# Performance work log

Measured on AMD Instinct MI355X. Metric: run time of the kernel, lower is better.

Reference implementation:

```python
import jax, jax.numpy as jnp
import numpy as np

D = 256      # dim
H = 8        # num_heads
HD = D // H  # head dim
P = 256      # patch_size
B = 4        # num clouds
L = 32768    # points per cloud (divisible by P)
N = B * L
MLP = int(D * 2.0)
PEH = max(32, D // 4)
EPS = 1e-5


def setup_inputs() -> dict:
    key = jax.random.key(0)
    ks = jax.random.split(key, 20)
    s = 0.02
    w = lambda k, shp: jax.random.normal(k, shp, jnp.float32) * s
    inp = {
        "feats": jax.random.normal(ks[0], (N, D), jnp.float32),
        "coord": jax.random.uniform(ks[1], (N, 3), jnp.float32),
        "lengths": jnp.full((B,), L, jnp.int32),
        # CoordPositionalEncoding: Linear(3,PEH) -> ReLU -> Linear(PEH,D)
        "pe_w1": w(ks[2], (3, PEH)), "pe_b1": jnp.zeros((PEH,), jnp.float32),
        "pe_w2": w(ks[3], (PEH, D)), "pe_b2": jnp.zeros((D,), jnp.float32),
        "pre_g": jnp.ones((D,), jnp.float32), "pre_b": jnp.zeros((D,), jnp.float32),
        # block: norm1 + MHA + norm2 + MLP
        "n1_g": jnp.ones((D,), jnp.float32), "n1_b": jnp.zeros((D,), jnp.float32),
        "wqkv": w(ks[4], (D, 3 * D)), "bqkv": jnp.zeros((3 * D,), jnp.float32),
        "wo": w(ks[5], (D, D)), "bo": jnp.zeros((D,), jnp.float32),
        "n2_g": jnp.ones((D,), jnp.float32), "n2_b": jnp.zeros((D,), jnp.float32),
        "m_w1": w(ks[6], (D, MLP)), "m_b1": jnp.zeros((MLP,), jnp.float32),
        "m_w2": w(ks[7], (MLP, D)), "m_b2": jnp.zeros((D,), jnp.float32),
        # global_gate: Linear(2D,D)->ReLU->Linear(D,D)->Sigmoid
        "gg_w1": w(ks[8], (2 * D, D)), "gg_b1": jnp.zeros((D,), jnp.float32),
        "gg_w2": w(ks[9], (D, D)), "gg_b2": jnp.zeros((D,), jnp.float32),
        # fuse: Linear(2D,D)->ReLU->Linear(D,D)
        "f_w1": w(ks[10], (2 * D, D)), "f_b1": jnp.zeros((D,), jnp.float32),
        "f_w2": w(ks[11], (D, D)), "f_b2": jnp.zeros((D,), jnp.float32),
    }
    return inp


def _ln(x, g, b):
    m = x.mean(-1, keepdims=True)
    v = jnp.mean((x - m) ** 2, -1, keepdims=True)
    return (x - m) * jax.lax.rsqrt(v + EPS) * g + b


def _sgca(feats, coord, lengths,
          pe_w1, pe_b1, pe_w2, pe_b2, pre_g, pre_b,
          n1_g, n1_b, wqkv, bqkv, wo, bo, n2_g, n2_b,
          m_w1, m_b1, m_w2, m_b2,
          gg_w1, gg_b1, gg_w2, gg_b2, f_w1, f_b1, f_w2, f_b2):
    Bn = lengths.shape[0]
    Ln = feats.shape[0] // Bn  # equal-length clouds

    def cloud(f, c):  # f: [L, D], c: [L, 3]
        # positional encoding (per-cloud centered / max-abs scaled coords)
        cc = c - c.mean(0, keepdims=True)
        scale = jnp.clip(jnp.abs(cc).max(0, keepdims=True), 1e-6)
        pe = jax.nn.relu((cc / scale) @ pe_w1 + pe_b1) @ pe_w2 + pe_b2
        x = _ln(f + pe, pre_g, pre_b)
        # serialization order from min-max normalized coords
        cn = c - c.min(0, keepdims=True)
        cn = cn / jnp.clip(cn.max(0, keepdims=True), 1e-6)
        key = cn[:, 0] + 2.17 * cn[:, 1] + 3.31 * cn[:, 2]
        order = jnp.argsort(key)
        xs = x[order].reshape(-1, P, D)  # [NP, P, D] block-diagonal windows
        # attention block (pre-norm MHA + residual)
        h = _ln(xs, n1_g, n1_b)
        qkv = h @ wqkv + bqkv
        q = qkv[..., :D].reshape(-1, P, H, HD)
        k = qkv[..., D:2 * D].reshape(-1, P, H, HD)
        v = qkv[..., 2 * D:].reshape(-1, P, H, HD)
        scores = jnp.einsum('nphd,nqhd->nhpq', q, k) / np.sqrt(HD).astype(np.float32)
        a = jax.nn.softmax(scores, axis=-1)
        o = jnp.einsum('nhpq,nqhd->nphd', a, v).reshape(-1, P, D)
        xs = xs + (o @ wo + bo)
        # MLP + residual
        xs = xs + (jax.nn.gelu(_ln(xs, n2_g, n2_b) @ m_w1 + m_b1, approximate=False) @ m_w2 + m_b2)
        # undo serialization
        xo = xs.reshape(-1, D)[jnp.argsort(order)]
        # global token gate/fuse
        gt = jnp.broadcast_to(xo.mean(0, keepdims=True), xo.shape)
        gate = jax.nn.sigmoid(jax.nn.relu(jnp.concatenate([f, gt], -1) @ gg_w1 + gg_b1) @ gg_w2 + gg_b2)
        fused = jax.nn.relu(jnp.concatenate([xo, gt], -1) @ f_w1 + f_b1) @ f_w2 + f_b2
        return f + gate * fused

    out = jax.vmap(cloud)(feats.reshape(Bn, Ln, D), coord.reshape(Bn, Ln, 3))
    return out.reshape(-1, D)


def reference(feats, coord, lengths,
              pe_w1, pe_b1, pe_w2, pe_b2, pre_g, pre_b,
              n1_g, n1_b, wqkv, bqkv, wo, bo, n2_g, n2_b,
              m_w1, m_b1, m_w2, m_b2,
              gg_w1, gg_b1, gg_w2, gg_b2, f_w1, f_b1, f_w2, f_b2):
    return _sgca(feats, coord, lengths,
                 pe_w1, pe_b1, pe_w2, pe_b2, pre_g, pre_b,
                 n1_g, n1_b, wqkv, bqkv, wo, bo, n2_g, n2_b,
                 m_w1, m_b1, m_w2, m_b2,
                 gg_w1, gg_b1, gg_w2, gg_b2, f_w1, f_b1, f_w2, f_b2)
```

## Files before the change

### kernel.cpp

```cpp
#include <hip/hip_runtime.h>
#include <hip/hip_bf16.h>
#include <math.h>

#define D_DIM 256
#define NHEAD 8
#define HDIM 32
#define PATCH 256
#define NCLOUD 4
#define LPC 32768
#define NTOT (NCLOUD * LPC)
#define MLPD 512
#define PEHID 64
#define LN_EPS 1e-5f
#define NCHUNK 4
#define CROWS (NTOT / NCHUNK)

typedef unsigned long long u64;
typedef unsigned short u16;
typedef short bf16x8 __attribute__((ext_vector_type(8)));
typedef float f32x4 __attribute__((ext_vector_type(4)));

__device__ __forceinline__ u16 f2bf(float x) {
  unsigned u = __float_as_uint(x);
  u += 0x7fffu + ((u >> 16) & 1u);
  return (u16)(u >> 16);
}
__device__ __forceinline__ float bf2f(u16 u) {
  return __uint_as_float(((unsigned)u) << 16);
}

__device__ __forceinline__ void gload_lds16(const u16* g, u16* l) {
  __builtin_amdgcn_global_load_lds((const __attribute__((address_space(1))) void*)g,
                                   (__attribute__((address_space(3))) void*)l, 16, 0, 0);
}

__global__ __launch_bounds__(256) void stats_kernel(const float* __restrict__ coord,
                                                    float* __restrict__ stats) {
  const int c = blockIdx.x, t = threadIdx.x;
  float sm[3] = {0.f, 0.f, 0.f};
  float mn[3] = {1e30f, 1e30f, 1e30f};
  float mx[3] = {-1e30f, -1e30f, -1e30f};
  const float* cp = coord + (size_t)c * LPC * 3;
  for (int i = t; i < LPC; i += 256) {
#pragma unroll
    for (int a = 0; a < 3; a++) {
      float v = cp[(size_t)i * 3 + a];
      sm[a] += v;
      mn[a] = fminf(mn[a], v);
      mx[a] = fmaxf(mx[a], v);
    }
  }
  __shared__ float sb[256];
  float rsum[3], rmn[3], rmx[3];
#pragma unroll
  for (int a = 0; a < 3; a++) {
    sb[t] = sm[a]; __syncthreads();
    for (int s = 128; s > 0; s >>= 1) { if (t < s) sb[t] += sb[t + s]; __syncthreads(); }
    rsum[a] = sb[0]; __syncthreads();
    sb[t] = mn[a]; __syncthreads();
    for (int s = 128; s > 0; s >>= 1) { if (t < s) sb[t] = fminf(sb[t], sb[t + s]); __syncthreads(); }
    rmn[a] = sb[0]; __syncthreads();
    sb[t] = mx[a]; __syncthreads();
    for (int s = 128; s > 0; s >>= 1) { if (t < s) sb[t] = fmaxf(sb[t], sb[t + s]); __syncthreads(); }
    rmx[a] = sb[0]; __syncthreads();
  }
  if (t == 0) {
    float* st = stats + c * 16;
#pragma unroll
    for (int a = 0; a < 3; a++) {
      float mean = rsum[a] / (float)LPC;
      st[a] = mean;
      st[3 + a] = fmaxf(fmaxf(rmx[a] - mean, mean - rmn[a]), 1e-6f);
      st[6 + a] = rmn[a];
      st[9 + a] = fmaxf(rmx[a] - rmn[a], 1e-6f);
    }
  }
}

__global__ __launch_bounds__(256) void key_kernel(const float* __restrict__ coord,
                                                  const float* __restrict__ stats,
                                                  u64* __restrict__ keys) {
#pragma clang fp contract(off)
  const int g = blockIdx.x * 256 + threadIdx.x;
  const int c = g >> 15;
  const float* st = stats + c * 16;
  float k0 = (coord[(size_t)g * 3 + 0] - st[6]) / st[9];
  float k1 = (coord[(size_t)g * 3 + 1] - st[7]) / st[10];
  float k2 = (coord[(size_t)g * 3 + 2] - st[8]) / st[11];
  float key = k0 + 2.17f * k1;
  key = key + 3.31f * k2;
  keys[g] = ((u64)__float_as_uint(key) << 32) | (unsigned)(g & (LPC - 1));
}

__global__ __launch_bounds__(1024) void sort_local_kernel(u64* __restrict__ keys) {
  __shared__ u64 s[4096];
  const int base = blockIdx.x * 4096;
  const int t = threadIdx.x;
  for (int i = t; i < 4096; i += 1024) s[i] = keys[base + i];
  __syncthreads();
  for (int k = 2; k <= 4096; k <<= 1) {
    for (int j = k >> 1; j > 0; j >>= 1) {
      for (int p = t; p < 2048; p += 1024) {
        int i = ((p & ~(j - 1)) << 1) | (p & (j - 1));
        int l = i | j;
        bool asc = (((base + i) & (LPC - 1)) & k) == 0;
        u64 a = s[i], bb = s[l];
        if (asc ? (a > bb) : (a < bb)) { s[i] = bb; s[l] = a; }
      }
      __syncthreads();
    }
  }
  for (int i = t; i < 4096; i += 1024) keys[base + i] = s[i];
}

__global__ __launch_bounds__(256) void sort_global_kernel(u64* __restrict__ keys, int k, int j) {
  int p = blockIdx.x * 256 + threadIdx.x;
  int i = ((p & ~(j - 1)) << 1) | (p & (j - 1));
  int l = i | j;
  bool asc = ((i & (LPC - 1)) & k) == 0;
  u64 a = keys[i], b = keys[l];
  if (asc ? (a > b) : (a < b)) { keys[i] = b; keys[l] = a; }
}

__global__ __launch_bounds__(1024) void sort_finish_kernel(u64* __restrict__ keys, int k) {
  __shared__ u64 s[4096];
  const int base = blockIdx.x * 4096;
  const int t = threadIdx.x;
  for (int i = t; i < 4096; i += 1024) s[i] = keys[base + i];
  __syncthreads();
  for (int j = 2048; j > 0; j >>= 1) {
    for (int p = t; p < 2048; p += 1024) {
      int i = ((p & ~(j - 1)) << 1) | (p & (j - 1));
      int l = i | j;
      bool asc = (((base + i) & (LPC - 1)) & k) == 0;
      u64 a = s[i], bb = s[l];
      if (asc ? (a > bb) : (a < bb)) { s[i] = bb; s[l] = a; }
    }
    __syncthreads();
  }
  for (int i = t; i < 4096; i += 1024) keys[base + i] = s[i];
}

__global__ __launch_bounds__(256) void rank_kernel(const u64* __restrict__ keys,
                                                   int* __restrict__ order,
                                                   int* __restrict__ rank) {
  const int g = blockIdx.x * 256 + threadIdx.x;
  const int src = (int)(unsigned)(keys[g] & 0xffffffffULL) + (g & ~(LPC - 1));
  order[g] = src;
  rank[src] = g;
}

__global__ __launch_bounds__(256) void wtrans_kernel(const float* __restrict__ src,
                                                     u16* __restrict__ dst, int R, int C) {
  __shared__ float t[32][33];
  const int bx = blockIdx.x * 32, by = blockIdx.y * 32;
  const int lc = threadIdx.x & 31, lr = threadIdx.x >> 5;
  for (int i = 0; i < 32; i += 8) t[lr + i][lc] = src[(size_t)(by + lr + i) * C + bx + lc];
  __syncthreads();
  for (int i = 0; i < 32; i += 8)
    dst[(size_t)(bx + lr + i) * R + by + lc] = f2bf(t[lc][lr + i]);
}

__global__ __launch_bounds__(256) void h_kernel(const float* __restrict__ coord,
                                                const float* __restrict__ stats,
                                                const float* __restrict__ pw1,
                                                const float* __restrict__ pb1,
                                                u16* __restrict__ H) {
  const int idx = blockIdx.x * 256 + threadIdx.x;
  const int row = idx >> 6, j = idx & 63;
  const int c = row >> 15;
  const float* st = stats + c * 16;
  float s0 = (coord[(size_t)row * 3 + 0] - st[0]) / st[3];
  float s1 = (coord[(size_t)row * 3 + 1] - st[1]) / st[4];
  float s2 = (coord[(size_t)row * 3 + 2] - st[2]) / st[5];
  float h = pb1[j] + s0 * pw1[j] + s1 * pw1[64 + j] + s2 * pw1[128 + j];
  H[idx] = f2bf(fmaxf(h, 0.f));
}

__global__ __launch_bounds__(256) void add_ln_kernel(const float* __restrict__ feats,
                                                     const u16* __restrict__ pe,
                                                     const int* __restrict__ rank,
                                                     const float* __restrict__ g,
                                                     const float* __restrict__ b,
                                                     float* __restrict__ xs) {
  const int row = blockIdx.x * 4 + (threadIdx.x >> 6);
  const int lane = threadIdx.x & 63;
  float4 f = *(const float4*)(feats + (size_t)row * 256 + lane * 4);
  ushort4 p = *(const ushort4*)(pe + (size_t)row * 256 + lane * 4);
  float v0 = f.x + bf2f(p.x), v1 = f.y + bf2f(p.y);
  float v2 = f.z + bf2f(p.z), v3 = f.w + bf2f(p.w);
  float s = v0 + v1 + v2 + v3;
#pragma unroll
  for (int o = 32; o > 0; o >>= 1) s += __shfl_xor(s, o);
  float mean = s * (1.f / 256.f);
  float d0 = v0 - mean, d1 = v1 - mean, d2 = v2 - mean, d3 = v3 - mean;
  float ss = d0 * d0 + d1 * d1 + d2 * d2 + d3 * d3;
#pragma unroll
  for (int o = 32; o > 0; o >>= 1) ss += __shfl_xor(ss, o);
  float inv = 1.f / sqrtf(ss * (1.f / 256.f) + LN_EPS);
  float4 gv = *(const float4*)(g + lane * 4);
  float4 bv = *(const float4*)(b + lane * 4);
  int dst = rank[row];
  float4 o4;
  o4.x = d0 * inv * gv.x + bv.x; o4.y = d1 * inv * gv.y + bv.y;
  o4.z = d2 * inv * gv.z + bv.z; o4.w = d3 * inv * gv.w + bv.w;
  *(float4*)(xs + (size_t)dst * 256 + lane * 4) = o4;
}

__global__ __launch_bounds__(256) void ln_bf16_kernel(const float* __restrict__ in,
                                                      const float* __restrict__ g,
                                                      const float* __restrict__ b,
                                                      u16* __restrict__ out) {
  const int row = blockIdx.x * 4 + (threadIdx.x >> 6);
  const int lane = threadIdx.x & 63;
  float4 v = *(const float4*)(in + (size_t)row * 256 + lane * 4);
  float s = v.x + v.y + v.z + v.w;
#pragma unroll
  for (int o = 32; o > 0; o >>= 1) s += __shfl_xor(s, o);
  float mean = s * (1.f / 256.f);
  float d0 = v.x - mean, d1 = v.y - mean, d2 = v.z - mean, d3 = v.w - mean;
  float ss = d0 * d0 + d1 * d1 + d2 * d2 + d3 * d3;
#pragma unroll
  for (int o = 32; o > 0; o >>= 1) ss += __shfl_xor(ss, o);
  float inv = 1.f / sqrtf(ss * (1.f / 256.f) + LN_EPS);
  float4 gv = *(const float4*)(g + lane * 4);
  float4 bv = *(const float4*)(b + lane * 4);
  ushort4 o4;
  o4.x = f2bf(d0 * inv * gv.x + bv.x); o4.y = f2bf(d1 * inv * gv.y + bv.y);
  o4.z = f2bf(d2 * inv * gv.z + bv.z); o4.w = f2bf(d3 * inv * gv.w + bv.w);
  *(ushort4*)(out + (size_t)row * 256 + lane * 4) = o4;
}

template <int K, int ACT, int MODE, bool EXTRA>
__global__ __launch_bounds__(256, 4) void mfma_gemm(const u16* __restrict__ A,
                                                    const u16* __restrict__ Wt,
                                                    const float* __restrict__ bias,
                                                    const float* __restrict__ extra,
                                                    void* __restrict__ Cout, int Ko) {
  __shared__ __align__(16) u16 Al[128 * 32];
  __shared__ __align__(16) u16 Bl[128 * 32];
  const int tid = threadIdx.x;
  const int lane = tid & 63, wave = tid >> 6;
  const int wr = wave >> 1, wc = wave & 1;
  const int l15 = lane & 15, l4 = lane >> 4;
  const size_t row0 = (size_t)blockIdx.y * 128;
  const int col0 = blockIdx.x * 128;
  const int q0 = wave * 64 + lane;
  const int q1 = q0 + 256;
  const u16* gA0 = A + (row0 + (q0 >> 2)) * K + (q0 & 3) * 8;
  const u16* gA1 = A + (row0 + (q1 >> 2)) * K + (q1 & 3) * 8;
  const u16* gB0 = Wt + (size_t)(col0 + (q0 >> 2)) * K + (q0 & 3) * 8;
  const u16* gB1 = Wt + (size_t)(col0 + (q1 >> 2)) * K + (q1 & 3) * 8;
  u16* lA0 = Al + wave * 512;
  u16* lA1 = Al + 2048 + wave * 512;
  u16* lB0 = Bl + wave * 512;
  u16* lB1 = Bl + 2048 + wave * 512;
  f32x4 acc[4][4];
#pragma unroll
  for (int i = 0; i < 4; i++)
#pragma unroll
    for (int j = 0; j < 4; j++) acc[i][j] = f32x4{0.f, 0.f, 0.f, 0.f};
#pragma unroll 1
  for (int k0 = 0; k0 < K; k0 += 32) {
    gload_lds16(gA0 + k0, lA0);
    gload_lds16(gA1 + k0, lA1);
    gload_lds16(gB0 + k0, lB0);
    gload_lds16(gB1 + k0, lB1);
    __syncthreads();
    bf16x8 af[4], bfr[4];
#pragma unroll
    for (int rb = 0; rb < 4; rb++)
      af[rb] = *(const bf16x8*)&Al[(wr * 64 + rb * 16 + l15) * 32 + l4 * 8];
#pragma unroll
    for (int cb = 0; cb < 4; cb++)
      bfr[cb] = *(const bf16x8*)&Bl[(wc * 64 + cb * 16 + l15) * 32 + l4 * 8];
#pragma unroll
    for (int rb = 0; rb < 4; rb++)
#pragma unroll
      for (int cb = 0; cb < 4; cb++)
        acc[rb][cb] = __builtin_amdgcn_mfma_f32_16x16x32_bf16(af[rb], bfr[cb], acc[rb][cb], 0, 0, 0);
    __syncthreads();
  }
#pragma unroll
  for (int rb = 0; rb < 4; rb++)
#pragma unroll
    for (int cb = 0; cb < 4; cb++)
#pragma unroll
      for (int r = 0; r < 4; r++) {
        size_t row = row0 + wr * 64 + rb * 16 + l4 * 4 + r;
        int col = col0 + wc * 64 + cb * 16 + l15;
        float v = acc[rb][cb][r] + bias[col];
        if (EXTRA) v += extra[((int)(row >> 15)) * 256 + col];
        if (ACT == 1) v = fmaxf(v, 0.f);
        else if (ACT == 2) v = 0.5f * v * (1.f + erff(v * 0.70710678118654752440f));
        else if (ACT == 3) v = 1.f / (1.f + __expf(-v));
        size_t o = row * (size_t)Ko + col;
        if (MODE == 0) ((float*)Cout)[o] = v;
        else if (MODE == 1) ((float*)Cout)[o] += v;
        else ((u16*)Cout)[o] = f2bf(v);
      }
}

template <int K, int EPI>
__global__ __launch_bounds__(256, 3) void mfma_row_gemm(const u16* __restrict__ A,
                                                        const u16* __restrict__ Wt,
                                                        const float* __restrict__ bias,
                                                        float* __restrict__ xs,
                                                        u16* __restrict__ hout,
                                                        const int* __restrict__ order,
                                                        const float* __restrict__ g,
                                                        const float* __restrict__ b) {
  __shared__ __align__(16) u16 Al[64 * 32];
  __shared__ __align__(16) u16 Bl[256 * 32];
  __shared__ float reds[2][4][64];
  const int tid = threadIdx.x;
  const int lane = tid & 63, wave = tid >> 6;
  const int l15 = lane & 15, l4 = lane >> 4;
  const size_t row0 = (size_t)blockIdx.x * 64;
  const u16* gA = A + (row0 + (tid >> 2)) * K + (tid & 3) * 8;
  u16* lA = Al + wave * 512;
  const u16* gB[4];
  u16* lB[4];
#pragma unroll
  for (int s = 0; s < 4; s++) {
    int q = s * 256 + tid;
    gB[s] = Wt + (size_t)(q >> 2) * K + (q & 3) * 8;
    lB[s] = Bl + s * 2048 + wave * 512;
  }
  f32x4 acc[4][4];
#pragma unroll
  for (int i = 0; i < 4; i++)
#pragma unroll
    for (int j = 0; j < 4; j++) acc[i][j] = f32x4{0.f, 0.f, 0.f, 0.f};
#pragma unroll 1
  for (int k0 = 0; k0 < K; k0 += 32) {
    gload_lds16(gA + k0, lA);
#pragma unroll
    for (int s = 0; s < 4; s++) gload_lds16(gB[s] + k0, lB[s]);
    __syncthreads();
    bf16x8 af[4], bfr[4];
#pragma unroll
    for (int rb = 0; rb < 4; rb++)
      af[rb] = *(const bf16x8*)&Al[(rb * 16 + l15) * 32 + l4 * 8];
#pragma unroll
    for (int cb = 0; cb < 4; cb++)
      bfr[cb] = *(const bf16x8*)&Bl[(wave * 64 + cb * 16 + l15) * 32 + l4 * 8];
#pragma unroll
    for (int rb = 0; rb < 4; rb++)
#pragma unroll
      for (int cb = 0; cb < 4; cb++)
        acc[rb][cb] = __builtin_amdgcn_mfma_f32_16x16x32_bf16(af[rb], bfr[cb], acc[rb][cb], 0, 0, 0);
    __syncthreads();
  }
#pragma unroll
  for (int rb = 0; rb < 4; rb++)
#pragma unroll
    for (int cb = 0; cb < 4; cb++)
#pragma unroll
      for (int r = 0; r < 4; r++) {
        size_t row = row0 + rb * 16 + l4 * 4 + r;
        int col = wave * 64 + cb * 16 + l15;
        size_t o = row * 256 + col;
        float t = xs[o] + acc[rb][cb][r] + bias[col];
        xs[o] = t;
        acc[rb][cb][r] = t;
      }
  if (EPI == 1) {
    float ps[4][4];
#pragma unroll
    for (int rb = 0; rb < 4; rb++)
#pragma unroll
      for (int r = 0; r < 4; r++) {
        float v = acc[rb][0][r] + acc[rb][1][r] + acc[rb][2][r] + acc[rb][3][r];
#pragma unroll
        for (int oo = 1; oo < 16; oo <<= 1) v += __shfl_xor(v, oo);
        ps[rb][r] = v;
      }
    if (l15 == 0)
#pragma unroll
      for (int rb = 0; rb < 4; rb++)
#pragma unroll
        for (int r = 0; r < 4; r++) reds[0][wave][rb * 16 + l4 * 4 + r] = ps[rb][r];
    __syncthreads();
    float mean[4][4];
#pragma unroll
    for (int rb = 0; rb < 4; rb++)
#pragma unroll
      for (int r = 0; r < 4; r++) {
        int ri = rb * 16 + l4 * 4 + r;
        mean[rb][r] = (reds[0][0][ri] + reds[0][1][ri] + reds[0][2][ri] + reds[0][3][ri]) *
                      (1.f / 256.f);
      }
#pragma unroll
    for (int rb = 0; rb < 4; rb++)
#pragma unroll
      for (int r = 0; r < 4; r++) {
        float d0 = acc[rb][0][r] - mean[rb][r], d1 = acc[rb][1][r] - mean[rb][r];
        float d2 = acc[rb][2][r] - mean[rb][r], d3 = acc[rb][3][r] - mean[rb][r];
        float v = d0 * d0 + d1 * d1 + d2 * d2 + d3 * d3;
#pragma unroll
        for (int oo = 1; oo < 16; oo <<= 1) v += __shfl_xor(v, oo);
        ps[rb][r] = v;
      }
    if (l15 == 0)
#pragma unroll
      for (int rb = 0; rb < 4; rb++)
#pragma unroll
        for (int r = 0; r < 4; r++) reds[1][wave][rb * 16 + l4 * 4 + r] = ps[rb][r];
    __syncthreads();
#pragma unroll
    for (int rb = 0; rb < 4; rb++)
#pragma unroll
      for (int r = 0; r < 4; r++) {
        int ri = rb * 16 + l4 * 4 + r;
        float var = (reds[1][0][ri] + reds[1][1][ri] + reds[1][2][ri] + reds[1][3][ri]) *
                    (1.f / 256.f);
        float inv = 1.f / sqrtf(var + LN_EPS);
        size_t row = row0 + ri;
#pragma unroll
        for (int cb = 0; cb < 4; cb++) {
          int col = wave * 64 + cb * 16 + l15;
          hout[row * 256 + col] =
              f2bf((acc[rb][cb][r] - mean[rb][r]) * inv * g[col] + b[col]);
        }
      }
  } else {
#pragma unroll
    for (int rb = 0; rb < 4; rb++)
#pragma unroll
      for (int r = 0; r < 4; r++) {
        size_t row = row0 + rb * 16 + l4 * 4 + r;
        size_t dst = (size_t)order[row];
#pragma unroll
        for (int cb = 0; cb < 4; cb++) {
          int col = wave * 64 + cb * 16 + l15;
          hout[dst * 256 + col] = f2bf(acc[rb][cb][r]);
        }
      }
  }
}

__global__ __launch_bounds__(256, 3) void tail_kernel(
    const float* __restrict__ feats, const u16* __restrict__ xobf,
    const u16* __restrict__ ggw1T, const u16* __restrict__ fw1T,
    const u16* __restrict__ ggw2T, const u16* __restrict__ fw2T,
    const float* __restrict__ ggt, const float* __restrict__ fgt,
    const float* __restrict__ b1g, const float* __restrict__ b1f,
    const float* __restrict__ b2g, const float* __restrict__ b2f,
    float* __restrict__ out) {
  __shared__ __align__(16) u16 g1l[32 * 264];
  __shared__ __align__(16) u16 u1l[32 * 264];
  __shared__ __align__(16) u16 Bst[256 * 32];
  __shared__ __align__(16) u16 Ast[32 * 32];
  const int tid = threadIdx.x;
  const int lane = tid & 63, wave = tid >> 6;
  const int l15 = lane & 15, l4 = lane >> 4;
  const size_t row0 = (size_t)blockIdx.x * 32;
  const int cloud = (int)(row0 >> 15);
  f32x4 acc[2][4];
#pragma unroll
  for (int i = 0; i < 2; i++)
#pragma unroll
    for (int j = 0; j < 4; j++) acc[i][j] = f32x4{0.f, 0.f, 0.f, 0.f};
#pragma unroll 1
  for (int k0 = 0; k0 < 256; k0 += 32) {
#pragma unroll
    for (int s = 0; s < 4; s++) {
      int q = s * 256 + tid;
      gload_lds16(ggw1T + (size_t)(q >> 2) * 256 + k0 + (q & 3) * 8,
                  Bst + s * 2048 + wave * 512);
    }
    {
      int r = tid >> 3, c4 = (tid & 7) * 4;
      float4 v = *(const float4*)(feats + (row0 + r) * 256 + k0 + c4);
      ushort4 o4; o4.x = f2bf(v.x); o4.y = f2bf(v.y); o4.z = f2bf(v.z); o4.w = f2bf(v.w);
      *(ushort4*)&Ast[r * 32 + c4] = o4;
    }
    __syncthreads();
    bf16x8 af[2];
#pragma unroll
    for (int rb = 0; rb < 2; rb++)
      af[rb] = *(const bf16x8*)&Ast[(rb * 16 + l15) * 32 + l4 * 8];
#pragma unroll
    for (int cb = 0; cb < 4; cb++) {
      bf16x8 bf = *(const bf16x8*)&Bst[(wave * 64 + cb * 16 + l15) * 32 + l4 * 8];
#pragma unroll
      for (int rb = 0; rb < 2; rb++)
        acc[rb][cb] = __builtin_amdgcn_mfma_f32_16x16x32_bf16(af[rb], bf, acc[rb][cb], 0, 0, 0);
    }
    __syncthreads();
  }
#pragma unroll
  for (int rb = 0; rb < 2; rb++)
#pragma unroll
    for (int cb = 0; cb < 4; cb++)
#pragma unroll
      for (int r = 0; r < 4; r++) {
        int row = rb * 16 + l4 * 4 + r;
        int col = wave * 64 + cb * 16 + l15;
        float v = acc[rb][cb][r] + b1g[col] + ggt[cloud * 256 + col];
        g1l[row * 264 + col] = f2bf(fmaxf(v, 0.f));
      }
#pragma unroll
  for (int i = 0; i < 2; i++)
#pragma unroll
    for (int j = 0; j < 4; j++) acc[i][j] = f32x4{0.f, 0.f, 0.f, 0.f};
#pragma unroll 1
  for (int k0 = 0; k0 < 256; k0 += 32) {
    __syncthreads();
#pragma unroll
    for (int s = 0; s < 4; s++) {
      int q = s * 256 + tid;
      gload_lds16(fw1T + (size_t)(q >> 2) * 256 + k0 + (q & 3) * 8,
                  Bst + s * 2048 + wave * 512);
    }
    if (tid < 128) {
      int q = tid;
      gload_lds16(xobf + (row0 + (q >> 2)) * 256 + k0 + (q & 3) * 8, Ast + wave * 512);
    }
    __syncthreads();
    bf16x8 af[2];
#pragma unroll
    for (int rb = 0; rb < 2; rb++)
      af[rb] = *(const bf16x8*)&Ast[(rb * 16 + l15) * 32 + l4 * 8];
#pragma unroll
    for (int cb = 0; cb < 4; cb++) {
      bf16x8 bf = *(const bf16x8*)&Bst[(wave * 64 + cb * 16 + l15) * 32 + l4 * 8];
#pragma unroll
      for (int rb = 0; rb < 2; rb++)
        acc[rb][cb] = __builtin_amdgcn_mfma_f32_16x16x32_bf16(af[rb], bf, acc[rb][cb], 0, 0, 0);
    }
  }
#pragma unroll
  for (int rb = 0; rb < 2; rb++)
#pragma unroll
    for (int cb = 0; cb < 4; cb++)
#pragma unroll
      for (int r = 0; r < 4; r++) {
        int row = rb * 16 + l4 * 4 + r;
        int col = wave * 64 + cb * 16 + l15;
        float v = acc[rb][cb][r] + b1f[col] + fgt[cloud * 256 + col];
        u1l[row * 264 + col] = f2bf(fmaxf(v, 0.f));
      }
#pragma unroll
  for (int i = 0; i < 2; i++)
#pragma unroll
    for (int j = 0; j < 4; j++) acc[i][j] = f32x4{0.f, 0.f, 0.f, 0.f};
#pragma unroll 1
  for (int k0 = 0; k0 < 256; k0 += 32) {
    __syncthreads();
#pragma unroll
    for (int s = 0; s < 4; s++) {
      int q = s * 256 + tid;
      gload_lds16(ggw2T + (size_t)(q >> 2) * 256 + k0 + (q & 3) * 8,
                  Bst + s * 2048 + wave * 512);
    }
    __syncthreads();
    bf16x8 af[2];
#pragma unroll
    for (int rb = 0; rb < 2; rb++)
      af[rb] = *(const bf16x8*)&g1l[(rb * 16 + l15) * 264 + k0 + l4 * 8];
#pragma unroll
    for (int cb = 0; cb < 4; cb++) {
      bf16x8 bf = *(const bf16x8*)&Bst[(wave * 64 + cb * 16 + l15) * 32 + l4 * 8];
#pragma unroll
      for (int rb = 0; rb < 2; rb++)
        acc[rb][cb] = __builtin_amdgcn_mfma_f32_16x16x32_bf16(af[rb], bf, acc[rb][cb], 0, 0, 0);
    }
  }
  float sg[2][4][4];
#pragma unroll
  for (int rb = 0; rb < 2; rb++)
#pragma unroll
    for (int cb = 0; cb < 4; cb++)
#pragma unroll
      for (int r = 0; r < 4; r++) {
        int col = wave * 64 + cb * 16 + l15;
        sg[rb][cb][r] = 1.f / (1.f + __expf(-(acc[rb][cb][r] + b2g[col])));
      }
#pragma unroll
  for (int i = 0; i < 2; i++)
#pragma unroll
    for (int j = 0; j < 4; j++) acc[i][j] = f32x4{0.f, 0.f, 0.f, 0.f};
#pragma unroll 1
  for (int k0 = 0; k0 < 256; k0 += 32) {
    __syncthreads();
#pragma unroll
    for (int s = 0; s < 4; s++) {
      int q = s * 256 + tid;
      gload_lds16(fw2T + (size_t)(q >> 2) * 256 + k0 + (q & 3) * 8,
                  Bst + s * 2048 + wave * 512);
    }
    __syncthreads();
    bf16x8 af[2];
#pragma unroll
    for (int rb = 0; rb < 2; rb++)
      af[rb] = *(const bf16x8*)&u1l[(rb * 16 + l15) * 264 + k0 + l4 * 8];
#pragma unroll
    for (int cb = 0; cb < 4; cb++) {
      bf16x8 bf = *(const bf16x8*)&Bst[(wave * 64 + cb * 16 + l15) * 32 + l4 * 8];
#pragma unroll
      for (int rb = 0; rb < 2; rb++)
        acc[rb][cb] = __builtin_amdgcn_mfma_f32_16x16x32_bf16(af[rb], bf, acc[rb][cb], 0, 0, 0);
    }
  }
#pragma unroll
  for (int rb = 0; rb < 2; rb++)
#pragma unroll
    for (int cb = 0; cb < 4; cb++)
#pragma unroll
      for (int r = 0; r < 4; r++) {
        size_t row = row0 + rb * 16 + l4 * 4 + r;
        int col = wave * 64 + cb * 16 + l15;
        size_t o = row * 256 + col;
        out[o] = feats[o] + sg[rb][cb][r] * (acc[rb][cb][r] + b2f[col]);
      }
}

__global__ __launch_bounds__(256, 3) void attn_mfma_kernel(const u16* __restrict__ qkv,
                                                           u16* __restrict__ ao) {
  __shared__ __align__(16) u16 VT[32 * 264];
  __shared__ __align__(16) u16 Pl[4][16 * 264];
  const int w = blockIdx.x, h = blockIdx.y;
  const int tid = threadIdx.x;
  const int lane = tid & 63, wave = tid >> 6;
  const int l15 = lane & 15, l4 = lane >> 4;
  const size_t base = (size_t)w * PATCH;
  {
    const u16* vrow = qkv + (base + tid) * 768 + 512 + h * HDIM;
#pragma unroll
    for (int d4 = 0; d4 < 8; d4++) {
      ushort4 v4 = *(const ushort4*)(vrow + d4 * 4);
      VT[(d4 * 4 + 0) * 264 + tid] = v4.x;
      VT[(d4 * 4 + 1) * 264 + tid] = v4.y;
      VT[(d4 * 4 + 2) * 264 + tid] = v4.z;
      VT[(d4 * 4 + 3) * 264 + tid] = v4.w;
    }
  }
  __syncthreads();
  u16* Pw = &Pl[wave][0];
  const float scale = 0.17677669529663687f;
  const f32x4 zero = {0.f, 0.f, 0.f, 0.f};
  for (int qt = 0; qt < 4; qt++) {
    const int qbase = wave * 64 + qt * 16;
    bf16x8 qf = *(const bf16x8*)(qkv + (base + qbase + l15) * 768 + h * HDIM + l4 * 8);
    f32x4 s[16];
#pragma unroll
    for (int kt = 0; kt < 16; kt++) {
      bf16x8 kf = *(const bf16x8*)(qkv + (base + kt * 16 + l15) * 768 + 256 + h * HDIM + l4 * 8);
      s[kt] = __builtin_amdgcn_mfma_f32_16x16x32_bf16(kf, qf, zero, 0, 0, 0);
    }
    float m = -1e30f;
#pragma unroll
    for (int kt = 0; kt < 16; kt++)
#pragma unroll
      for (int r = 0; r < 4; r++) { s[kt][r] *= scale; m = fmaxf(m, s[kt][r]); }
    m = fmaxf(m, __shfl_xor(m, 16));
    m = fmaxf(m, __shfl_xor(m, 32));
    float lsum = 0.f;
#pragma unroll
    for (int kt = 0; kt < 16; kt++) {
      float p0 = __expf(s[kt][0] - m), p1 = __expf(s[kt][1] - m);
      float p2 = __expf(s[kt][2] - m), p3 = __expf(s[kt][3] - m);
      lsum += (p0 + p1) + (p2 + p3);
      ushort4 pw4;
      pw4.x = f2bf(p0); pw4.y = f2bf(p1); pw4.z = f2bf(p2); pw4.w = f2bf(p3);
      *(ushort4*)&Pw[l15 * 264 + kt * 16 + l4 * 4] = pw4;
    }
    lsum += __shfl_xor(lsum, 16);
    lsum += __shfl_xor(lsum, 32);
    f32x4 o0 = zero, o1 = zero;
#pragma unroll
    for (int kc = 0; kc < 8; kc++) {
      bf16x8 pf = *(const bf16x8*)&Pw[l15 * 264 + kc * 32 + l4 * 8];
      bf16x8 va = *(const bf16x8*)&VT[l15 * 264 + kc * 32 + l4 * 8];
      bf16x8 vb = *(const bf16x8*)&VT[(16 + l15) * 264 + kc * 32 + l4 * 8];
      o0 = __builtin_amdgcn_mfma_f32_16x16x32_bf16(va, pf, o0, 0, 0, 0);
      o1 = __builtin_amdgcn_mfma_f32_16x16x32_bf16(vb, pf, o1, 0, 0, 0);
    }
    float inv = 1.f / lsum;
    u16* op = ao + (base + qbase + l15) * D_DIM + h * HDIM;
    ushort4 w0, w1;
    w0.x = f2bf(o0[0] * inv); w0.y = f2bf(o0[1] * inv);
    w0.z = f2bf(o0[2] * inv); w0.w = f2bf(o0[3] * inv);
    w1.x = f2bf(o1[0] * inv); w1.y = f2bf(o1[1] * inv);
    w1.z = f2bf(o1[2] * inv); w1.w = f2bf(o1[3] * inv);
    *(ushort4*)(op + l4 * 4) = w0;
    *(ushort4*)(op + 16 + l4 * 4) = w1;
  }
}

__global__ __launch_bounds__(256) void gt_partial_kernel(const float* __restrict__ xs,
                                                         float* __restrict__ part) {
  const int s = blockIdx.x, c = blockIdx.y;
  const int t = threadIdx.x;
  float acc = 0.f;
  const size_t base = (size_t)c * LPC + (size_t)s * 256;
  for (int r = 0; r < 256; r++) acc += xs[(base + r) * D_DIM + t];
  part[(size_t)(c * 128 + s) * D_DIM + t] = acc;
}

__global__ __launch_bounds__(256) void gt_reduce_kernel(const float* __restrict__ part,
                                                        float* __restrict__ gt) {
  const int c = blockIdx.x, t = threadIdx.x;
  float s = 0.f;
  for (int i = 0; i < 128; i++) s += part[(size_t)(c * 128 + i) * D_DIM + t];
  gt[c * D_DIM + t] = s * (1.f / (float)LPC);
}

__global__ __launch_bounds__(256) void pervec_kernel(const float* __restrict__ gt,
                                                     const float* __restrict__ ggw1,
                                                     const float* __restrict__ fw1,
                                                     float* __restrict__ ggt,
                                                     float* __restrict__ fgt) {
  const int c = blockIdx.x, which = blockIdx.y;
  const int t = threadIdx.x;
  const float* W = which ? fw1 : ggw1;
  float* o = which ? fgt : ggt;
  __shared__ float g[D_DIM];
  g[t] = gt[c * D_DIM + t];
  __syncthreads();
  float acc = 0.f;
#pragma unroll 8
  for (int k = 0; k < D_DIM; k++) acc += g[k] * W[(size_t)(256 + k) * D_DIM + t];
  o[c * D_DIM + t] = acc;
}

extern "C" void kernel_launch(void* const* d_in, const int* in_sizes, int n_in,
                              void* d_out, int out_size, void* d_ws, size_t ws_size,
                              hipStream_t stream) {
  const float* feats = (const float*)d_in[0];
  const float* coord = (const float*)d_in[1];
  const float* pe_w1 = (const float*)d_in[3];
  const float* pe_b1 = (const float*)d_in[4];
  const float* pe_w2 = (const float*)d_in[5];
  const float* pe_b2 = (const float*)d_in[6];
  const float* pre_g = (const float*)d_in[7];
  const float* pre_b = (const float*)d_in[8];
  const float* n1_g = (const float*)d_in[9];
  const float* n1_b = (const float*)d_in[10];
  const float* wqkv = (const float*)d_in[11];
  const float* bqkv = (const float*)d_in[12];
  const float* wo = (const float*)d_in[13];
  const float* bo = (const float*)d_in[14];
  const float* n2_g = (const float*)d_in[15];
  const float* n2_b = (const float*)d_in[16];
  const float* m_w1 = (const float*)d_in[17];
  const float* m_b1 = (const float*)d_in[18];
  const float* m_w2 = (const float*)d_in[19];
  const float* m_b2 = (const float*)d_in[20];
  const float* gg_w1 = (const float*)d_in[21];
  const float* gg_b1 = (const float*)d_in[22];
  const float* gg_w2 = (const float*)d_in[23];
  const float* gg_b2 = (const float*)d_in[24];
  const float* f_w1 = (const float*)d_in[25];
  const float* f_b1 = (const float*)d_in[26];
  const float* f_w2 = (const float*)d_in[27];
  const float* f_b2 = (const float*)d_in[28];
  float* out = (float*)d_out;

  char* ws = (char*)d_ws;
  float* xs = (float*)(ws);
  u16* hbuf = (u16*)(ws + 134217728);
  u16* qkvchunk = (u16*)(ws + 201326592);
  u16* aochunk = (u16*)(ws + 251658240);
  u16* tbuf = (u16*)(ws + 268435456);
  u16* Hbuf = (u16*)(ws + 268435456);
  u16* xobf = (u16*)(ws + 201326592);
  size_t off = 301989888;
  u64* keybuf = (u64*)(ws + off); off += (size_t)NTOT * 8;
  int* orderbuf = (int*)(ws + off); off += (size_t)NTOT * 4;
  int* rankbuf = (int*)(ws + off); off += (size_t)NTOT * 4;
  float* statsbuf = (float*)(ws + off); off += 4096;
  float* gtpart = (float*)(ws + off); off += (size_t)NCLOUD * 128 * D_DIM * 4;
  float* gtbuf = (float*)(ws + off); off += 4096;
  float* ggtbuf = (float*)(ws + off); off += 4096;
  float* fgtbuf = (float*)(ws + off); off += 4096;
  u16* wqkvT = (u16*)(ws + off); off += 768 * 256 * 2;
  u16* woT = (u16*)(ws + off); off += 256 * 256 * 2;
  u16* mw1T = (u16*)(ws + off); off += 512 * 256 * 2;
  u16* mw2T = (u16*)(ws + off); off += 256 * 512 * 2;
  u16* ggw1T = (u16*)(ws + off); off += 256 * 256 * 2;
  u16* ggw2T = (u16*)(ws + off); off += 256 * 256 * 2;
  u16* fw1T = (u16*)(ws + off); off += 256 * 256 * 2;
  u16* fw2T = (u16*)(ws + off); off += 256 * 256 * 2;
  u16* pw2T = (u16*)(ws + off); off += 64 * 256 * 2;

  stats_kernel<<<NCLOUD, 256, 0, stream>>>(coord, statsbuf);
  key_kernel<<<NTOT / 256, 256, 0, stream>>>(coord, statsbuf, keybuf);
  sort_local_kernel<<<NTOT / 4096, 1024, 0, stream>>>(keybuf);
  for (int k = 8192; k <= 32768; k <<= 1) {
    for (int j = k >> 1; j >= 4096; j >>= 1)
      sort_global_kernel<<<NTOT / 512, 256, 0, stream>>>(keybuf, k, j);
    sort_finish_kernel<<<NTOT / 4096, 1024, 0, stream>>>(keybuf, k);
  }
  rank_kernel<<<NTOT / 256, 256, 0, stream>>>(keybuf, orderbuf, rankbuf);
  wtrans_kernel<<<dim3(24, 8), 256, 0, stream>>>(wqkv, wqkvT, 256, 768);
  wtrans_kernel<<<dim3(8, 8), 256, 0, stream>>>(wo, woT, 256, 256);
  wtrans_kernel<<<dim3(16, 8), 256, 0, stream>>>(m_w1, mw1T, 256, 512);
  wtrans_kernel<<<dim3(8, 16), 256, 0, stream>>>(m_w2, mw2T, 512, 256);
  wtrans_kernel<<<dim3(8, 8), 256, 0, stream>>>(gg_w1, ggw1T, 256, 256);
  wtrans_kernel<<<dim3(8, 8), 256, 0, stream>>>(gg_w2, ggw2T, 256, 256);
  wtrans_kernel<<<dim3(8, 8), 256, 0, stream>>>(f_w1, fw1T, 256, 256);
  wtrans_kernel<<<dim3(8, 8), 256, 0, stream>>>(f_w2, fw2T, 256, 256);
  wtrans_kernel<<<dim3(8, 2), 256, 0, stream>>>(pe_w2, pw2T, 64, 256);
  h_kernel<<<NTOT * 64 / 256, 256, 0, stream>>>(coord, statsbuf, pe_w1, pe_b1, Hbuf);
  mfma_gemm<64, 0, 2, false><<<dim3(2, NTOT / 128), 256, 0, stream>>>(
      Hbuf, pw2T, pe_b2, nullptr, hbuf, 256);
  add_ln_kernel<<<NTOT / 4, 256, 0, stream>>>(feats, hbuf, rankbuf, pre_g, pre_b, xs);
  ln_bf16_kernel<<<NTOT / 4, 256, 0, stream>>>(xs, n1_g, n1_b, hbuf);
  for (int ch = 0; ch < NCHUNK; ch++) {
    const size_t ro = (size_t)ch * CROWS;
    mfma_gemm<256, 0, 2, false><<<dim3(6, CROWS / 128), 256, 0, stream>>>(
        hbuf + ro * 256, wqkvT, bqkv, nullptr, qkvchunk, 768);
    attn_mfma_kernel<<<dim3(CROWS / PATCH, NHEAD), 256, 0, stream>>>(qkvchunk, aochunk);
    mfma_row_gemm<256, 1><<<CROWS / 64, 256, 0, stream>>>(
        aochunk, woT, bo, xs + ro * 256, hbuf + ro * 256, nullptr, n2_g, n2_b);
  }
  for (int ch = 0; ch < NCHUNK; ch++) {
    const size_t ro = (size_t)ch * CROWS;
    mfma_gemm<256, 2, 2, false><<<dim3(MLPD / 128, CROWS / 128), 256, 0, stream>>>(
        hbuf + ro * 256, mw1T, m_b1, nullptr, tbuf, 512);
    mfma_row_gemm<512, 2><<<CROWS / 64, 256, 0, stream>>>(
        tbuf, mw2T, m_b2, xs + ro * 256, xobf, orderbuf + ro, nullptr, nullptr);
  }
  gt_partial_kernel<<<dim3(128, NCLOUD), 256, 0, stream>>>(xs, gtpart);
  gt_reduce_kernel<<<NCLOUD, 256, 0, stream>>>(gtpart, gtbuf);
  pervec_kernel<<<dim3(NCLOUD, 2), 256, 0, stream>>>(gtbuf, gg_w1, f_w1, ggtbuf, fgtbuf);
  tail_kernel<<<NTOT / 32, 256, 0, stream>>>(feats, xobf, ggw1T, fw1T, ggw2T, fw2T,
                                             ggtbuf, fgtbuf, gg_b1, f_b1, gg_b2, f_b2, out);
  (void)in_sizes; (void)n_in; (void)out_size; (void)ws_size;
}
```

Baseline: 1.359 ms.

## Load tail GEMM operands directly from global memory, dropping LDS staging

The four chained GEMMs in the tail kernel now read weight and activation fragments straight from global memory into registers instead of staging them through shared-memory tiles. This removes the per-k-step barriers and the LDS buffers, lowering LDS use so more blocks may fit per CU. A single barrier is added before the second-stage GEMMs so the intermediate LDS tiles are complete before use. In exchange, each wave issues uncoalesced 16-byte global loads with no prefetch and relies on L2/L1 caching of the shared weights.

```diff
diff --git a/kernel.cpp b/kernel.cpp
--- a/kernel.cpp
+++ b/kernel.cpp
@@ -450,45 +450,39 @@
     float* __restrict__ out) {
   __shared__ __align__(16) u16 g1l[32 * 264];
   __shared__ __align__(16) u16 u1l[32 * 264];
-  __shared__ __align__(16) u16 Bst[256 * 32];
-  __shared__ __align__(16) u16 Ast[32 * 32];
   const int tid = threadIdx.x;
   const int lane = tid & 63, wave = tid >> 6;
   const int l15 = lane & 15, l4 = lane >> 4;
   const size_t row0 = (size_t)blockIdx.x * 32;
   const int cloud = (int)(row0 >> 15);
   f32x4 acc[2][4];
+
 #pragma unroll
   for (int i = 0; i < 2; i++)
 #pragma unroll
     for (int j = 0; j < 4; j++) acc[i][j] = f32x4{0.f, 0.f, 0.f, 0.f};
 #pragma unroll 1
   for (int k0 = 0; k0 < 256; k0 += 32) {
-#pragma unroll
-    for (int s = 0; s < 4; s++) {
-      int q = s * 256 + tid;
-      gload_lds16(ggw1T + (size_t)(q >> 2) * 256 + k0 + (q & 3) * 8,
-                  Bst + s * 2048 + wave * 512);
-    }
-    {
-      int r = tid >> 3, c4 = (tid & 7) * 4;
-      float4 v = *(const float4*)(feats + (row0 + r) * 256 + k0 + c4);
-      ushort4 o4; o4.x = f2bf(v.x); o4.y = f2bf(v.y); o4.z = f2bf(v.z); o4.w = f2bf(v.w);
-      *(ushort4*)&Ast[r * 32 + c4] = o4;
-    }
-    __syncthreads();
     bf16x8 af[2];
 #pragma unroll
-    for (int rb = 0; rb < 2; rb++)
-      af[rb] = *(const bf16x8*)&Ast[(rb * 16 + l15) * 32 + l4 * 8];
+    for (int rb = 0; rb < 2; rb++) {
+      const float* fp = feats + (row0 + rb * 16 + l15) * 256 + k0 + l4 * 8;
+      float4 v0 = *(const float4*)(fp);
+      float4 v1 = *(const float4*)(fp + 4);
+      ushort4 h0, h1;
+      h0.x = f2bf(v0.x); h0.y = f2bf(v0.y); h0.z = f2bf(v0.z); h0.w = f2bf(v0.w);
+      h1.x = f2bf(v1.x); h1.y = f2bf(v1.y); h1.z = f2bf(v1.z); h1.w = f2bf(v1.w);
+      union { ushort4 u4[2]; bf16x8 b8; } cvt;
+      cvt.u4[0] = h0; cvt.u4[1] = h1;
+      af[rb] = cvt.b8;
+    }
 #pragma unroll
     for (int cb = 0; cb < 4; cb++) {
-      bf16x8 bf = *(const bf16x8*)&Bst[(wave * 64 + cb * 16 + l15) * 32 + l4 * 8];
+      bf16x8 bf = *(const bf16x8*)(ggw1T + (size_t)(wave * 64 + cb * 16 + l15) * 256 + k0 + l4 * 8);
 #pragma unroll
       for (int rb = 0; rb < 2; rb++)
         acc[rb][cb] = __builtin_amdgcn_mfma_f32_16x16x32_bf16(af[rb], bf, acc[rb][cb], 0, 0, 0);
     }
-    __syncthreads();
   }
 #pragma unroll
   for (int rb = 0; rb < 2; rb++)
@@ -507,25 +501,13 @@
     for (int j = 0; j < 4; j++) acc[i][j] = f32x4{0.f, 0.f, 0.f, 0.f};
 #pragma unroll 1
   for (int k0 = 0; k0 < 256; k0 += 32) {
-    __syncthreads();
-#pragma unroll
-    for (int s = 0; s < 4; s++) {
-      int q = s * 256 + tid;
-      gload_lds16(fw1T + (size_t)(q >> 2) * 256 + k0 + (q & 3) * 8,
-                  Bst + s * 2048 + wave * 512);
-    }
-    if (tid < 128) {
-      int q = tid;
-      gload_lds16(xobf + (row0 + (q >> 2)) * 256 + k0 + (q & 3) * 8, Ast + wave * 512);
-    }
-    __syncthreads();
     bf16x8 af[2];
 #pragma unroll
     for (int rb = 0; rb < 2; rb++)
-      af[rb] = *(const bf16x8*)&Ast[(rb * 16 + l15) * 32 + l4 * 8];
+      af[rb] = *(const bf16x8*)(xobf + (row0 + rb * 16 + l15) * 256 + k0 + l4 * 8);
 #pragma unroll
     for (int cb = 0; cb < 4; cb++) {
-      bf16x8 bf = *(const bf16x8*)&Bst[(wave * 64 + cb * 16 + l15) * 32 + l4 * 8];
+      bf16x8 bf = *(const bf16x8*)(fw1T + (size_t)(wave * 64 + cb * 16 + l15) * 256 + k0 + l4 * 8);
 #pragma unroll
       for (int rb = 0; rb < 2; rb++)
         acc[rb][cb] = __builtin_amdgcn_mfma_f32_16x16x32_bf16(af[rb], bf, acc[rb][cb], 0, 0, 0);
@@ -542,27 +524,20 @@
         float v = acc[rb][cb][r] + b1f[col] + fgt[cloud * 256 + col];
         u1l[row * 264 + col] = f2bf(fmaxf(v, 0.f));
       }
+  __syncthreads();
 #pragma unroll
   for (int i = 0; i < 2; i++)
 #pragma unroll
     for (int j = 0; j < 4; j++) acc[i][j] = f32x4{0.f, 0.f, 0.f, 0.f};
 #pragma unroll 1
   for (int k0 = 0; k0 < 256; k0 += 32) {
-    __syncthreads();
-#pragma unroll
-    for (int s = 0; s < 4; s++) {
-      int q = s * 256 + tid;
-      gload_lds16(ggw2T + (size_t)(q >> 2) * 256 + k0 + (q & 3) * 8,
-                  Bst + s * 2048 + wave * 512);
-    }
-    __syncthreads();
     bf16x8 af[2];
 #pragma unroll
     for (int rb = 0; rb < 2; rb++)
       af[rb] = *(const bf16x8*)&g1l[(rb * 16 + l15) * 264 + k0 + l4 * 8];
 #pragma unroll
     for (int cb = 0; cb < 4; cb++) {
-      bf16x8 bf = *(const bf16x8*)&Bst[(wave * 64 + cb * 16 + l15) * 32 + l4 * 8];
+      bf16x8 bf = *(const bf16x8*)(ggw2T + (size_t)(wave * 64 + cb * 16 + l15) * 256 + k0 + l4 * 8);
 #pragma unroll
       for (int rb = 0; rb < 2; rb++)
         acc[rb][cb] = __builtin_amdgcn_mfma_f32_16x16x32_bf16(af[rb], bf, acc[rb][cb], 0, 0, 0);
@@ -584,21 +559,13 @@
     for (int j = 0; j < 4; j++) acc[i][j] = f32x4{0.f, 0.f, 0.f, 0.f};
 #pragma unroll 1
   for (int k0 = 0; k0 < 256; k0 += 32) {
-    __syncthreads();
-#pragma unroll
-    for (int s = 0; s < 4; s++) {
-      int q = s * 256 + tid;
-      gload_lds16(fw2T + (size_t)(q >> 2) * 256 + k0 + (q & 3) * 8,
-                  Bst + s * 2048 + wave * 512);
-    }
-    __syncthreads();
     bf16x8 af[2];
 #pragma unroll
     for (int rb = 0; rb < 2; rb++)
       af[rb] = *(const bf16x8*)&u1l[(rb * 16 + l15) * 264 + k0 + l4 * 8];
 #pragma unroll
     for (int cb = 0; cb < 4; cb++) {
-      bf16x8 bf = *(const bf16x8*)&Bst[(wave * 64 + cb * 16 + l15) * 32 + l4 * 8];
+      bf16x8 bf = *(const bf16x8*)(fw2T + (size_t)(wave * 64 + cb * 16 + l15) * 256 + k0 + l4 * 8);
 #pragma unroll
       for (int rb = 0; rb < 2; rb++)
         acc[rb][cb] = __builtin_amdgcn_mfma_f32_16x16x32_bf16(af[rb], bf, acc[rb][cb], 0, 0, 0);
```

Result: slower. 1.481 ms (+9.0%).
